# Performance work log

Measured on AMD Instinct MI355X. Metric: run time of the kernel, lower is better.

Reference implementation:

```python
import jax, jax.numpy as jnp
import numpy as np

NUM_STREAMS = 4
DIM = 256
SINKHORN_ITERS = 10
SINKHORN_TAU = 0.05


def sinkhorn_log(logits, num_iters=SINKHORN_ITERS, tau=SINKHORN_TAU):
    n = logits.shape[-1]
    z = logits / tau
    log_marginal = -jnp.log(jnp.asarray(float(n), dtype=logits.dtype))

    def body(carry, _):
        u, v = carry
        u = log_marginal - jax.scipy.special.logsumexp(z + v[None, :], axis=1)
        v = log_marginal - jax.scipy.special.logsumexp(z + u[:, None], axis=0)
        return (u, v), None

    u0 = jnp.zeros((n,), dtype=z.dtype)
    v0 = jnp.zeros((n,), dtype=z.dtype)
    (u, v), _ = jax.lax.scan(body, (u0, v0), None, length=num_iters)
    return jnp.exp(z + u[:, None] + v[None, :]) * n


def setup_inputs() -> dict:
    key = jax.random.key(0)
    k_res, k_w = jax.random.split(key)
    B = 65536
    residuals = jax.random.normal(k_res, (B, NUM_STREAMS, DIM), dtype=jnp.float32)
    # h_res_logits: -8 everywhere, 0 on diagonal (as in __init__)
    h_res_logits = jnp.full((NUM_STREAMS, NUM_STREAMS), -8.0, dtype=jnp.float32)
    h_res_logits = h_res_logits.at[jnp.arange(NUM_STREAMS), jnp.arange(NUM_STREAMS)].set(0.0)
    # h_pre_logits: -8 everywhere, 0 at init_residual_index=0
    h_pre_logits = jnp.full((NUM_STREAMS,), -8.0, dtype=jnp.float32).at[0].set(0.0)
    h_post_logits = jnp.zeros((NUM_STREAMS,), dtype=jnp.float32)
    # branch Linear(dim, dim, bias=False): weight (out, in), y = x @ W.T
    bound = 1.0 / np.sqrt(DIM)
    W_branch = jax.random.uniform(k_w, (DIM, DIM), dtype=jnp.float32, minval=-bound, maxval=bound)
    return {
        "residuals": residuals,
        "h_res_logits": h_res_logits,
        "h_pre_logits": h_pre_logits,
        "h_post_logits": h_post_logits,
        "W_branch": W_branch,
    }


def reference(residuals, h_res_logits, h_pre_logits, h_post_logits, W_branch):
    # residuals: (B, S, D)
    h_res = sinkhorn_log(h_res_logits)                     # (S, S) doubly-stochastic * n
    h_pre = jax.nn.softmax(h_pre_logits)                   # (S,)
    h_post = jax.nn.softmax(h_post_logits)                 # (S,)
    residuals_mixed = jnp.einsum('st,bsd->btd', h_res, residuals)
    branch_input = jnp.einsum('s,bsd->bd', h_pre, residuals)
    branch_output = branch_input @ W_branch.T              # (B, D)
    depth_out = jnp.einsum('bd,s->bsd', branch_output, h_post)
    return residuals_mixed + depth_out
```

## Files before the change

### kernel.cpp

```cpp
#include <hip/hip_runtime.h>

#define NSTREAMS 4
#define DIM 256
#define BM 16
#define NTHREADS 1024
#define TILES 16

typedef __attribute__((ext_vector_type(8))) short short8;
typedef __attribute__((ext_vector_type(4))) float f32x4;

static __device__ __forceinline__ int2 f2bf4(float4 v) {
    unsigned int lo, hi;
    asm("v_cvt_pk_bf16_f32 %0, %1, %2" : "=v"(lo) : "v"(v.x), "v"(v.y));
    asm("v_cvt_pk_bf16_f32 %0, %1, %2" : "=v"(hi) : "v"(v.z), "v"(v.w));
    int2 r; r.x = (int)lo; r.y = (int)hi;
    return r;
}

static __device__ __forceinline__ float rfl(float x) {
    int i = __builtin_amdgcn_readfirstlane(__builtin_bit_cast(int, x));
    return __builtin_bit_cast(float, i);
}

static __device__ __forceinline__ void barrier_lgkm() {
    asm volatile("s_waitcnt lgkmcnt(0)\n\ts_barrier" ::: "memory");
}

__global__ __launch_bounds__(NTHREADS, 1) void fused_kernel(
    const float* __restrict__ res,
    const float* __restrict__ Wb,
    const float* __restrict__ hres_l,
    const float* __restrict__ hpre_l,
    const float* __restrict__ hpost_l,
    float* __restrict__ out)
{
    __shared__ __align__(16) short bi_lds[2][BM][DIM + 8];
    __shared__ __align__(16) float bo_lds[BM][DIM + 4];

    const int t  = threadIdx.x;
    const int w  = t >> 6;
    const int l  = t & 63;
    const int lr = l & 15;
    const int lk = l >> 4;

    const long tile0 = (long)blockIdx.x * TILES;
    const long tstride = (long)BM * (NSTREAMS * DIM);
    const float* rl0 = res + (tile0 * BM + w) * (long)(NSTREAMS * DIM) + l * 4;
    float* ob0 = out + (tile0 * BM + w) * (long)(4 * DIM) + l * 4;
    const int dcol = w * 16 + lr;

    float4 A0, A1, A2, A3;
    A0 = *reinterpret_cast<const float4*>(rl0 + 0 * DIM);
    A1 = *reinterpret_cast<const float4*>(rl0 + 1 * DIM);
    A2 = *reinterpret_cast<const float4*>(rl0 + 2 * DIM);
    A3 = *reinterpret_cast<const float4*>(rl0 + 3 * DIM);

    const float4* wrow4 = reinterpret_cast<const float4*>(Wb + dcol * DIM);
    float4 wfa[8], wfb[8];
    #pragma unroll
    for (int kk = 0; kk < 8; ++kk) {
        wfa[kk] = wrow4[kk * 8 + lk * 2];
        wfb[kk] = wrow4[kk * 8 + lk * 2 + 1];
    }

    float hres[4][4];
    float hp0, hp1, hp2, hp3;
    float hq[4];
    {
        const int li = l & 15;
        float z = hres_l[li] * 20.0f;
        float uu = 0.f, vv = 0.f;
        const float logm = -logf(4.0f);
        #pragma unroll 1
        for (int it = 0; it < 10; ++it) {
            float tj = z + vv;
            float m = fmaxf(tj, __shfl_xor(tj, 1));
            m = fmaxf(m, __shfl_xor(m, 2));
            float e = expf(tj - m);
            float ss = e + __shfl_xor(e, 1);
            ss += __shfl_xor(ss, 2);
            uu = logm - (m + logf(ss));
            float ti2 = z + uu;
            float m2 = fmaxf(ti2, __shfl_xor(ti2, 4));
            m2 = fmaxf(m2, __shfl_xor(m2, 8));
            float e2 = expf(ti2 - m2);
            float s2 = e2 + __shfl_xor(e2, 4);
            s2 += __shfl_xor(s2, 8);
            vv = logm - (m2 + logf(s2));
        }
        float hval = expf(z + uu + vv) * 4.0f;
        #pragma unroll
        for (int s = 0; s < 4; ++s)
            #pragma unroll
            for (int tt = 0; tt < 4; ++tt)
                hres[s][tt] = rfl(__shfl(hval, s * 4 + tt));
        float p0 = hpre_l[0], p1 = hpre_l[1], p2 = hpre_l[2], p3 = hpre_l[3];
        float pm = fmaxf(fmaxf(p0, p1), fmaxf(p2, p3));
        float e0 = expf(p0 - pm), e1 = expf(p1 - pm), e2 = expf(p2 - pm), e3 = expf(p3 - pm);
        float es = e0 + e1 + e2 + e3;
        hp0 = rfl(e0 / es); hp1 = rfl(e1 / es); hp2 = rfl(e2 / es); hp3 = rfl(e3 / es);
        float q0 = hpost_l[0], q1 = hpost_l[1], q2 = hpost_l[2], q3 = hpost_l[3];
        float qm = fmaxf(fmaxf(q0, q1), fmaxf(q2, q3));
        float f0 = expf(q0 - qm), f1 = expf(q1 - qm), f2 = expf(q2 - qm), f3 = expf(q3 - qm);
        float fs = f0 + f1 + f2 + f3;
        hq[0] = rfl(f0 / fs); hq[1] = rfl(f1 / fs); hq[2] = rfl(f2 / fs); hq[3] = rfl(f3 / fs);
    }

    short8 wf[8];
    #pragma unroll
    for (int kk = 0; kk < 8; ++kk) {
        union { int4 i; short8 s; } u8;
        int2 lo = f2bf4(wfa[kk]);
        int2 hi = f2bf4(wfb[kk]);
        u8.i.x = lo.x; u8.i.y = lo.y; u8.i.z = hi.x; u8.i.w = hi.y;
        wf[kk] = u8.s;
    }

    {
        float4 bi;
        bi.x = hp0 * A0.x + hp1 * A1.x + hp2 * A2.x + hp3 * A3.x;
        bi.y = hp0 * A0.y + hp1 * A1.y + hp2 * A2.y + hp3 * A3.y;
        bi.z = hp0 * A0.z + hp1 * A1.z + hp2 * A2.z + hp3 * A3.z;
        bi.w = hp0 * A0.w + hp1 * A1.w + hp2 * A2.w + hp3 * A3.w;
        *reinterpret_cast<int2*>(&bi_lds[0][w][l * 4]) = f2bf4(bi);
    }
    float4 B0, B1, B2, B3;
    B0 = *reinterpret_cast<const float4*>(rl0 + tstride + 0 * DIM);
    B1 = *reinterpret_cast<const float4*>(rl0 + tstride + 1 * DIM);
    B2 = *reinterpret_cast<const float4*>(rl0 + tstride + 2 * DIM);
    B3 = *reinterpret_cast<const float4*>(rl0 + tstride + 3 * DIM);

    barrier_lgkm();

    for (int ti = 0; ti < TILES; ti += 2) {
        {
            f32x4 acc = {0.f, 0.f, 0.f, 0.f};
            #pragma unroll
            for (int kk = 0; kk < 8; ++kk) {
                short8 bfrag = *reinterpret_cast<const short8*>(&bi_lds[0][lr][kk * 32 + lk * 8]);
                acc = __builtin_amdgcn_mfma_f32_16x16x32_bf16(wf[kk], bfrag, acc, 0, 0, 0);
            }
            *reinterpret_cast<f32x4*>(&bo_lds[lr][(w << 4) + (lk << 2)]) = acc;
            barrier_lgkm();
            {
                f32x4 bo = *reinterpret_cast<const f32x4*>(&bo_lds[w][l * 4]);
                float* ob = ob0 + ti * (long)(BM * 4 * DIM);
                #pragma unroll
                for (int tt = 0; tt < 4; ++tt) {
                    float4 o;
                    o.x = hq[tt] * bo[0] + hres[0][tt] * A0.x + hres[1][tt] * A1.x + hres[2][tt] * A2.x + hres[3][tt] * A3.x;
                    o.y = hq[tt] * bo[1] + hres[0][tt] * A0.y + hres[1][tt] * A1.y + hres[2][tt] * A2.y + hres[3][tt] * A3.y;
                    o.z = hq[tt] * bo[2] + hres[0][tt] * A0.z + hres[1][tt] * A1.z + hres[2][tt] * A2.z + hres[3][tt] * A3.z;
                    o.w = hq[tt] * bo[3] + hres[0][tt] * A0.w + hres[1][tt] * A1.w + hres[2][tt] * A2.w + hres[3][tt] * A3.w;
                    *reinterpret_cast<float4*>(ob + tt * DIM) = o;
                }
            }
            if (ti + 2 < TILES) {
                const float* rb = rl0 + (ti + 2) * tstride;
                A0 = *reinterpret_cast<const float4*>(rb + 0 * DIM);
                A1 = *reinterpret_cast<const float4*>(rb + 1 * DIM);
                A2 = *reinterpret_cast<const float4*>(rb + 2 * DIM);
                A3 = *reinterpret_cast<const float4*>(rb + 3 * DIM);
            }
            __builtin_amdgcn_sched_barrier(0);
            {
                float4 bi;
                bi.x = hp0 * B0.x + hp1 * B1.x + hp2 * B2.x + hp3 * B3.x;
                bi.y = hp0 * B0.y + hp1 * B1.y + hp2 * B2.y + hp3 * B3.y;
                bi.z = hp0 * B0.z + hp1 * B1.z + hp2 * B2.z + hp3 * B3.z;
                bi.w = hp0 * B0.w + hp1 * B1.w + hp2 * B2.w + hp3 * B3.w;
                *reinterpret_cast<int2*>(&bi_lds[1][w][l * 4]) = f2bf4(bi);
            }
            barrier_lgkm();
        }
        {
            f32x4 acc = {0.f, 0.f, 0.f, 0.f};
            #pragma unroll
            for (int kk = 0; kk < 8; ++kk) {
                short8 bfrag = *reinterpret_cast<const short8*>(&bi_lds[1][lr][kk * 32 + lk * 8]);
                acc = __builtin_amdgcn_mfma_f32_16x16x32_bf16(wf[kk], bfrag, acc, 0, 0, 0);
            }
            *reinterpret_cast<f32x4*>(&bo_lds[lr][(w << 4) + (lk << 2)]) = acc;
            barrier_lgkm();
            {
                f32x4 bo = *reinterpret_cast<const f32x4*>(&bo_lds[w][l * 4]);
                float* ob = ob0 + (ti + 1) * (long)(BM * 4 * DIM);
                #pragma unroll
                for (int tt = 0; tt < 4; ++tt) {
                    float4 o;
                    o.x = hq[tt] * bo[0] + hres[0][tt] * B0.x + hres[1][tt] * B1.x + hres[2][tt] * B2.x + hres[3][tt] * B3.x;
                    o.y = hq[tt] * bo[1] + hres[0][tt] * B0.y + hres[1][tt] * B1.y + hres[2][tt] * B2.y + hres[3][tt] * B3.y;
                    o.z = hq[tt] * bo[2] + hres[0][tt] * B0.z + hres[1][tt] * B1.z + hres[2][tt] * B2.z + hres[3][tt] * B3.z;
                    o.w = hq[tt] * bo[3] + hres[0][tt] * B0.w + hres[1][tt] * B1.w + hres[2][tt] * B2.w + hres[3][tt] * B3.w;
                    *reinterpret_cast<float4*>(ob + tt * DIM) = o;
                }
            }
            if (ti + 3 < TILES) {
                const float* rb = rl0 + (ti + 3) * tstride;
                B0 = *reinterpret_cast<const float4*>(rb + 0 * DIM);
                B1 = *reinterpret_cast<const float4*>(rb + 1 * DIM);
                B2 = *reinterpret_cast<const float4*>(rb + 2 * DIM);
                B3 = *reinterpret_cast<const float4*>(rb + 3 * DIM);
            }
            __builtin_amdgcn_sched_barrier(0);
            if (ti + 2 < TILES) {
                float4 bi;
                bi.x = hp0 * A0.x + hp1 * A1.x + hp2 * A2.x + hp3 * A3.x;
                bi.y = hp0 * A0.y + hp1 * A1.y + hp2 * A2.y + hp3 * A3.y;
                bi.z = hp0 * A0.z + hp1 * A1.z + hp2 * A2.z + hp3 * A3.z;
                bi.w = hp0 * A0.w + hp1 * A1.w + hp2 * A2.w + hp3 * A3.w;
                *reinterpret_cast<int2*>(&bi_lds[0][w][l * 4]) = f2bf4(bi);
            }
            barrier_lgkm();
        }
    }
}

extern "C" void kernel_launch(void* const* d_in, const int* in_sizes, int n_in,
                              void* d_out, int out_size, void* d_ws, size_t ws_size,
                              hipStream_t stream) {
    const float* res     = (const float*)d_in[0];
    const float* hres_l  = (const float*)d_in[1];
    const float* hpre_l  = (const float*)d_in[2];
    const float* hpost_l = (const float*)d_in[3];
    const float* Wb      = (const float*)d_in[4];
    float* out = (float*)d_out;

    const int Btot = in_sizes[0] / (NSTREAMS * DIM);
    const int grid = Btot / (BM * TILES);

    fused_kernel<<<grid, NTHREADS, 0, stream>>>(
        res, Wb, hres_l, hpre_l, hpost_l, out);
}
```

Measured before the change: 114.4 us.

## Software-pipeline MFMA and epilogue with double-buffered output LDS to halve barriers

Double-buffers the branch-output LDS tile so the epilogue for tile i-1 runs in the same phase as the MFMA for tile i. This drops one block-wide barrier per tile. The residual-mix part of each output (hres times the four streams) is now computed early, when the residuals are loaded, and held in registers, so the epilogue only adds hq*bo. This adds about 32 live VGPRs (opA/opB) and LDS usage, which could raise register pressure in the 1024-thread block.

```diff
diff --git a/kernel.cpp b/kernel.cpp
--- a/kernel.cpp
+++ b/kernel.cpp
@@ -35,7 +35,7 @@
     float* __restrict__ out)
 {
     __shared__ __align__(16) short bi_lds[2][BM][DIM + 8];
-    __shared__ __align__(16) float bo_lds[BM][DIM + 4];
+    __shared__ __align__(16) float bo_lds[2][BM][DIM + 4];
 
     const int t  = threadIdx.x;
     const int w  = t >> 6;
@@ -116,6 +116,7 @@
         wf[kk] = u8.s;
     }
 
+    float4 opA[4], opB[4];
     {
         float4 bi;
         bi.x = hp0 * A0.x + hp1 * A1.x + hp2 * A2.x + hp3 * A3.x;
@@ -123,6 +124,13 @@
         bi.z = hp0 * A0.z + hp1 * A1.z + hp2 * A2.z + hp3 * A3.z;
         bi.w = hp0 * A0.w + hp1 * A1.w + hp2 * A2.w + hp3 * A3.w;
         *reinterpret_cast<int2*>(&bi_lds[0][w][l * 4]) = f2bf4(bi);
+        #pragma unroll
+        for (int tt = 0; tt < 4; ++tt) {
+            opA[tt].x = hres[0][tt] * A0.x + hres[1][tt] * A1.x + hres[2][tt] * A2.x + hres[3][tt] * A3.x;
+            opA[tt].y = hres[0][tt] * A0.y + hres[1][tt] * A1.y + hres[2][tt] * A2.y + hres[3][tt] * A3.y;
+            opA[tt].z = hres[0][tt] * A0.z + hres[1][tt] * A1.z + hres[2][tt] * A2.z + hres[3][tt] * A3.z;
+            opA[tt].w = hres[0][tt] * A0.w + hres[1][tt] * A1.w + hres[2][tt] * A2.w + hres[3][tt] * A3.w;
+        }
     }
     float4 B0, B1, B2, B3;
     B0 = *reinterpret_cast<const float4*>(rl0 + tstride + 0 * DIM);
@@ -134,27 +142,6 @@
 
     for (int ti = 0; ti < TILES; ti += 2) {
         {
-            f32x4 acc = {0.f, 0.f, 0.f, 0.f};
-            #pragma unroll
-            for (int kk = 0; kk < 8; ++kk) {
-                short8 bfrag = *reinterpret_cast<const short8*>(&bi_lds[0][lr][kk * 32 + lk * 8]);
-                acc = __builtin_amdgcn_mfma_f32_16x16x32_bf16(wf[kk], bfrag, acc, 0, 0, 0);
-            }
-            *reinterpret_cast<f32x4*>(&bo_lds[lr][(w << 4) + (lk << 2)]) = acc;
-            barrier_lgkm();
-            {
-                f32x4 bo = *reinterpret_cast<const f32x4*>(&bo_lds[w][l * 4]);
-                float* ob = ob0 + ti * (long)(BM * 4 * DIM);
-                #pragma unroll
-                for (int tt = 0; tt < 4; ++tt) {
-                    float4 o;
-                    o.x = hq[tt] * bo[0] + hres[0][tt] * A0.x + hres[1][tt] * A1.x + hres[2][tt] * A2.x + hres[3][tt] * A3.x;
-                    o.y = hq[tt] * bo[1] + hres[0][tt] * A0.y + hres[1][tt] * A1.y + hres[2][tt] * A2.y + hres[3][tt] * A3.y;
-                    o.z = hq[tt] * bo[2] + hres[0][tt] * A0.z + hres[1][tt] * A1.z + hres[2][tt] * A2.z + hres[3][tt] * A3.z;
-                    o.w = hq[tt] * bo[3] + hres[0][tt] * A0.w + hres[1][tt] * A1.w + hres[2][tt] * A2.w + hres[3][tt] * A3.w;
-                    *reinterpret_cast<float4*>(ob + tt * DIM) = o;
-                }
-            }
             if (ti + 2 < TILES) {
                 const float* rb = rl0 + (ti + 2) * tstride;
                 A0 = *reinterpret_cast<const float4*>(rb + 0 * DIM);
@@ -163,6 +150,28 @@
                 A3 = *reinterpret_cast<const float4*>(rb + 3 * DIM);
             }
             __builtin_amdgcn_sched_barrier(0);
+            if (ti > 0) {
+                f32x4 bo = *reinterpret_cast<const f32x4*>(&bo_lds[1][w][l * 4]);
+                float* ob = ob0 + (ti - 1) * (long)(BM * 4 * DIM);
+                #pragma unroll
+                for (int tt = 0; tt < 4; ++tt) {
+                    float4 o;
+                    o.x = opB[tt].x + hq[tt] * bo[0];
+                    o.y = opB[tt].y + hq[tt] * bo[1];
+                    o.z = opB[tt].z + hq[tt] * bo[2];
+                    o.w = opB[tt].w + hq[tt] * bo[3];
+                    *reinterpret_cast<float4*>(ob + tt * DIM) = o;
+                }
+            }
+            {
+                f32x4 acc = {0.f, 0.f, 0.f, 0.f};
+                #pragma unroll
+                for (int kk = 0; kk < 8; ++kk) {
+                    short8 bfrag = *reinterpret_cast<const short8*>(&bi_lds[0][lr][kk * 32 + lk * 8]);
+                    acc = __builtin_amdgcn_mfma_f32_16x16x32_bf16(wf[kk], bfrag, acc, 0, 0, 0);
+                }
+                *reinterpret_cast<f32x4*>(&bo_lds[0][lr][(w << 4) + (lk << 2)]) = acc;
+            }
             {
                 float4 bi;
                 bi.x = hp0 * B0.x + hp1 * B1.x + hp2 * B2.x + hp3 * B3.x;
@@ -170,31 +179,17 @@
                 bi.z = hp0 * B0.z + hp1 * B1.z + hp2 * B2.z + hp3 * B3.z;
                 bi.w = hp0 * B0.w + hp1 * B1.w + hp2 * B2.w + hp3 * B3.w;
                 *reinterpret_cast<int2*>(&bi_lds[1][w][l * 4]) = f2bf4(bi);
+                #pragma unroll
+                for (int tt = 0; tt < 4; ++tt) {
+                    opB[tt].x = hres[0][tt] * B0.x + hres[1][tt] * B1.x + hres[2][tt] * B2.x + hres[3][tt] * B3.x;
+                    opB[tt].y = hres[0][tt] * B0.y + hres[1][tt] * B1.y + hres[2][tt] * B2.y + hres[3][tt] * B3.y;
+                    opB[tt].z = hres[0][tt] * B0.z + hres[1][tt] * B1.z + hres[2][tt] * B2.z + hres[3][tt] * B3.z;
+                    opB[tt].w = hres[0][tt] * B0.w + hres[1][tt] * B1.w + hres[2][tt] * B2.w + hres[3][tt] * B3.w;
+                }
             }
             barrier_lgkm();
         }
         {
-            f32x4 acc = {0.f, 0.f, 0.f, 0.f};
-            #pragma unroll
-            for (int kk = 0; kk < 8; ++kk) {
-                short8 bfrag = *reinterpret_cast<const short8*>(&bi_lds[1][lr][kk * 32 + lk * 8]);
-                acc = __builtin_amdgcn_mfma_f32_16x16x32_bf16(wf[kk], bfrag, acc, 0, 0, 0);
-            }
-            *reinterpret_cast<f32x4*>(&bo_lds[lr][(w << 4) + (lk << 2)]) = acc;
-            barrier_lgkm();
-            {
-                f32x4 bo = *reinterpret_cast<const f32x4*>(&bo_lds[w][l * 4]);
-                float* ob = ob0 + (ti + 1) * (long)(BM * 4 * DIM);
-                #pragma unroll
-                for (int tt = 0; tt < 4; ++tt) {
-                    float4 o;
-                    o.x = hq[tt] * bo[0] + hres[0][tt] * B0.x + hres[1][tt] * B1.x + hres[2][tt] * B2.x + hres[3][tt] * B3.x;
-                    o.y = hq[tt] * bo[1] + hres[0][tt] * B0.y + hres[1][tt] * B1.y + hres[2][tt] * B2.y + hres[3][tt] * B3.y;
-                    o.z = hq[tt] * bo[2] + hres[0][tt] * B0.z + hres[1][tt] * B1.z + hres[2][tt] * B2.z + hres[3][tt] * B3.z;
-                    o.w = hq[tt] * bo[3] + hres[0][tt] * B0.w + hres[1][tt] * B1.w + hres[2][tt] * B2.w + hres[3][tt] * B3.w;
-                    *reinterpret_cast<float4*>(ob + tt * DIM) = o;
-                }
-            }
             if (ti + 3 < TILES) {
                 const float* rb = rl0 + (ti + 3) * tstride;
                 B0 = *reinterpret_cast<const float4*>(rb + 0 * DIM);
@@ -203,6 +198,28 @@
                 B3 = *reinterpret_cast<const float4*>(rb + 3 * DIM);
             }
             __builtin_amdgcn_sched_barrier(0);
+            {
+                f32x4 bo = *reinterpret_cast<const f32x4*>(&bo_lds[0][w][l * 4]);
+                float* ob = ob0 + ti * (long)(BM * 4 * DIM);
+                #pragma unroll
+                for (int tt = 0; tt < 4; ++tt) {
+                    float4 o;
+                    o.x = opA[tt].x + hq[tt] * bo[0];
+                    o.y = opA[tt].y + hq[tt] * bo[1];
+                    o.z = opA[tt].z + hq[tt] * bo[2];
+                    o.w = opA[tt].w + hq[tt] * bo[3];
+                    *reinterpret_cast<float4*>(ob + tt * DIM) = o;
+                }
+            }
+            {
+                f32x4 acc = {0.f, 0.f, 0.f, 0.f};
+                #pragma unroll
+                for (int kk = 0; kk < 8; ++kk) {
+                    short8 bfrag = *reinterpret_cast<const short8*>(&bi_lds[1][lr][kk * 32 + lk * 8]);
+                    acc = __builtin_amdgcn_mfma_f32_16x16x32_bf16(wf[kk], bfrag, acc, 0, 0, 0);
+                }
+                *reinterpret_cast<f32x4*>(&bo_lds[1][lr][(w << 4) + (lk << 2)]) = acc;
+            }
             if (ti + 2 < TILES) {
                 float4 bi;
                 bi.x = hp0 * A0.x + hp1 * A1.x + hp2 * A2.x + hp3 * A3.x;
@@ -210,8 +227,28 @@
                 bi.z = hp0 * A0.z + hp1 * A1.z + hp2 * A2.z + hp3 * A3.z;
                 bi.w = hp0 * A0.w + hp1 * A1.w + hp2 * A2.w + hp3 * A3.w;
                 *reinterpret_cast<int2*>(&bi_lds[0][w][l * 4]) = f2bf4(bi);
+                #pragma unroll
+                for (int tt = 0; tt < 4; ++tt) {
+                    opA[tt].x = hres[0][tt] * A0.x + hres[1][tt] * A1.x + hres[2][tt] * A2.x + hres[3][tt] * A3.x;
+                    opA[tt].y = hres[0][tt] * A0.y + hres[1][tt] * A1.y + hres[2][tt] * A2.y + hres[3][tt] * A3.y;
+                    opA[tt].z = hres[0][tt] * A0.z + hres[1][tt] * A1.z + hres[2][tt] * A2.z + hres[3][tt] * A3.z;
+                    opA[tt].w = hres[0][tt] * A0.w + hres[1][tt] * A1.w + hres[2][tt] * A2.w + hres[3][tt] * A3.w;
+                }
             }
             barrier_lgkm();
+        }
+    }
+    {
+        f32x4 bo = *reinterpret_cast<const f32x4*>(&bo_lds[1][w][l * 4]);
+        float* ob = ob0 + (TILES - 1) * (long)(BM * 4 * DIM);
+        #pragma unroll
+        for (int tt = 0; tt < 4; ++tt) {
+            float4 o;
+            o.x = opB[tt].x + hq[tt] * bo[0];
+            o.y = opB[tt].y + hq[tt] * bo[1];
+            o.z = opB[tt].z + hq[tt] * bo[2];
+            o.w = opB[tt].w + hq[tt] * bo[3];
+            *reinterpret_cast<float4*>(ob + tt * DIM) = o;
         }
     }
 }
```

Result: slower. 124.2 us (+8.6%).

## Drop register-resident weights and double buffering, raise occupancy with smaller tiles

Applied to the files above, without the earlier changes.

The kernel no longer preloads and converts the branch weight fragments into registers once per block. It now reloads them from global memory and converts them to bf16 inside every MFMA k-step. The two-stage register/LDS double-buffered pipeline becomes a simple single-buffer loop, TILES per block drops from 16 to 8 (twice the blocks), and launch bounds now ask for 8 blocks per CU instead of 1. The aim is to cut register pressure so more waves can hide memory latency, at the cost of redundant weight loads and conversions on every tile and no explicit prefetch overlap.

```diff
diff --git a/kernel.cpp b/kernel.cpp
--- a/kernel.cpp
+++ b/kernel.cpp
@@ -4,7 +4,7 @@
 #define DIM 256
 #define BM 16
 #define NTHREADS 1024
-#define TILES 16
+#define TILES 8
 
 typedef __attribute__((ext_vector_type(8))) short short8;
 typedef __attribute__((ext_vector_type(4))) float f32x4;
@@ -26,7 +26,7 @@
     asm volatile("s_waitcnt lgkmcnt(0)\n\ts_barrier" ::: "memory");
 }
 
-__global__ __launch_bounds__(NTHREADS, 1) void fused_kernel(
+__global__ __launch_bounds__(NTHREADS, 8) void fused_kernel(
     const float* __restrict__ res,
     const float* __restrict__ Wb,
     const float* __restrict__ hres_l,
@@ -34,7 +34,7 @@
     const float* __restrict__ hpost_l,
     float* __restrict__ out)
 {
-    __shared__ __align__(16) short bi_lds[2][BM][DIM + 8];
+    __shared__ __align__(16) short bi_lds[BM][DIM + 8];
     __shared__ __align__(16) float bo_lds[BM][DIM + 4];
 
     const int t  = threadIdx.x;
@@ -48,20 +48,7 @@
     const float* rl0 = res + (tile0 * BM + w) * (long)(NSTREAMS * DIM) + l * 4;
     float* ob0 = out + (tile0 * BM + w) * (long)(4 * DIM) + l * 4;
     const int dcol = w * 16 + lr;
-
-    float4 A0, A1, A2, A3;
-    A0 = *reinterpret_cast<const float4*>(rl0 + 0 * DIM);
-    A1 = *reinterpret_cast<const float4*>(rl0 + 1 * DIM);
-    A2 = *reinterpret_cast<const float4*>(rl0 + 2 * DIM);
-    A3 = *reinterpret_cast<const float4*>(rl0 + 3 * DIM);
-
     const float4* wrow4 = reinterpret_cast<const float4*>(Wb + dcol * DIM);
-    float4 wfa[8], wfb[8];
-    #pragma unroll
-    for (int kk = 0; kk < 8; ++kk) {
-        wfa[kk] = wrow4[kk * 8 + lk * 2];
-        wfb[kk] = wrow4[kk * 8 + lk * 2 + 1];
-    }
 
     float hres[4][4];
     float hp0, hp1, hp2, hp3;
@@ -106,112 +93,52 @@
         hq[0] = rfl(f0 / fs); hq[1] = rfl(f1 / fs); hq[2] = rfl(f2 / fs); hq[3] = rfl(f3 / fs);
     }
 
-    short8 wf[8];
-    #pragma unroll
-    for (int kk = 0; kk < 8; ++kk) {
-        union { int4 i; short8 s; } u8;
-        int2 lo = f2bf4(wfa[kk]);
-        int2 hi = f2bf4(wfb[kk]);
-        u8.i.x = lo.x; u8.i.y = lo.y; u8.i.z = hi.x; u8.i.w = hi.y;
-        wf[kk] = u8.s;
-    }
+    for (int ti = 0; ti < TILES; ++ti) {
+        const float* rb = rl0 + ti * tstride;
+        float4 R0 = *reinterpret_cast<const float4*>(rb + 0 * DIM);
+        float4 R1 = *reinterpret_cast<const float4*>(rb + 1 * DIM);
+        float4 R2 = *reinterpret_cast<const float4*>(rb + 2 * DIM);
+        float4 R3 = *reinterpret_cast<const float4*>(rb + 3 * DIM);
 
-    {
-        float4 bi;
-        bi.x = hp0 * A0.x + hp1 * A1.x + hp2 * A2.x + hp3 * A3.x;
-        bi.y = hp0 * A0.y + hp1 * A1.y + hp2 * A2.y + hp3 * A3.y;
-        bi.z = hp0 * A0.z + hp1 * A1.z + hp2 * A2.z + hp3 * A3.z;
-        bi.w = hp0 * A0.w + hp1 * A1.w + hp2 * A2.w + hp3 * A3.w;
-        *reinterpret_cast<int2*>(&bi_lds[0][w][l * 4]) = f2bf4(bi);
-    }
-    float4 B0, B1, B2, B3;
-    B0 = *reinterpret_cast<const float4*>(rl0 + tstride + 0 * DIM);
-    B1 = *reinterpret_cast<const float4*>(rl0 + tstride + 1 * DIM);
-    B2 = *reinterpret_cast<const float4*>(rl0 + tstride + 2 * DIM);
-    B3 = *reinterpret_cast<const float4*>(rl0 + tstride + 3 * DIM);
+        {
+            float4 bi;
+            bi.x = hp0 * R0.x + hp1 * R1.x + hp2 * R2.x + hp3 * R3.x;
+            bi.y = hp0 * R0.y + hp1 * R1.y + hp2 * R2.y + hp3 * R3.y;
+            bi.z = hp0 * R0.z + hp1 * R1.z + hp2 * R2.z + hp3 * R3.z;
+            bi.w = hp0 * R0.w + hp1 * R1.w + hp2 * R2.w + hp3 * R3.w;
+            *reinterpret_cast<int2*>(&bi_lds[w][l * 4]) = f2bf4(bi);
+        }
+        barrier_lgkm();
 
-    barrier_lgkm();
-
-    for (int ti = 0; ti < TILES; ti += 2) {
         {
             f32x4 acc = {0.f, 0.f, 0.f, 0.f};
             #pragma unroll
             for (int kk = 0; kk < 8; ++kk) {
-                short8 bfrag = *reinterpret_cast<const short8*>(&bi_lds[0][lr][kk * 32 + lk * 8]);
-                acc = __builtin_amdgcn_mfma_f32_16x16x32_bf16(wf[kk], bfrag, acc, 0, 0, 0);
+                short8 bfrag = *reinterpret_cast<const short8*>(&bi_lds[lr][kk * 32 + lk * 8]);
+                float4 wa = wrow4[kk * 8 + lk * 2];
+                float4 wb2 = wrow4[kk * 8 + lk * 2 + 1];
+                union { int4 i; short8 s; } u8;
+                int2 lo = f2bf4(wa);
+                int2 hi = f2bf4(wb2);
+                u8.i.x = lo.x; u8.i.y = lo.y; u8.i.z = hi.x; u8.i.w = hi.y;
+                acc = __builtin_amdgcn_mfma_f32_16x16x32_bf16(u8.s, bfrag, acc, 0, 0, 0);
             }
             *reinterpret_cast<f32x4*>(&bo_lds[lr][(w << 4) + (lk << 2)]) = acc;
-            barrier_lgkm();
-            {
-                f32x4 bo = *reinterpret_cast<const f32x4*>(&bo_lds[w][l * 4]);
-                float* ob = ob0 + ti * (long)(BM * 4 * DIM);
-                #pragma unroll
-                for (int tt = 0; tt < 4; ++tt) {
-                    float4 o;
-                    o.x = hq[tt] * bo[0] + hres[0][tt] * A0.x + hres[1][tt] * A1.x + hres[2][tt] * A2.x + hres[3][tt] * A3.x;
-                    o.y = hq[tt] * bo[1] + hres[0][tt] * A0.y + hres[1][tt] * A1.y + hres[2][tt] * A2.y + hres[3][tt] * A3.y;
-                    o.z = hq[tt] * bo[2] + hres[0][tt] * A0.z + hres[1][tt] * A1.z + hres[2][tt] * A2.z + hres[3][tt] * A3.z;
-                    o.w = hq[tt] * bo[3] + hres[0][tt] * A0.w + hres[1][tt] * A1.w + hres[2][tt] * A2.w + hres[3][tt] * A3.w;
-                    *reinterpret_cast<float4*>(ob + tt * DIM) = o;
-                }
+        }
+        barrier_lgkm();
+
+        {
+            f32x4 bo = *reinterpret_cast<const f32x4*>(&bo_lds[w][l * 4]);
+            float* ob = ob0 + ti * (long)(BM * 4 * DIM);
+            #pragma unroll
+            for (int tt = 0; tt < 4; ++tt) {
+                float4 o;
+                o.x = hq[tt] * bo[0] + hres[0][tt] * R0.x + hres[1][tt] * R1.x + hres[2][tt] * R2.x + hres[3][tt] * R3.x;
+                o.y = hq[tt] * bo[1] + hres[0][tt] * R0.y + hres[1][tt] * R1.y + hres[2][tt] * R2.y + hres[3][tt] * R3.y;
+                o.z = hq[tt] * bo[2] + hres[0][tt] * R0.z + hres[1][tt] * R1.z + hres[2][tt] * R2.z + hres[3][tt] * R3.z;
+                o.w = hq[tt] * bo[3] + hres[0][tt] * R0.w + hres[1][tt] * R1.w + hres[2][tt] * R2.w + hres[3][tt] * R3.w;
+                *reinterpret_cast<float4*>(ob + tt * DIM) = o;
             }
-            if (ti + 2 < TILES) {
-                const float* rb = rl0 + (ti + 2) * tstride;
-                A0 = *reinterpret_cast<const float4*>(rb + 0 * DIM);
-                A1 = *reinterpret_cast<const float4*>(rb + 1 * DIM);
-                A2 = *reinterpret_cast<const float4*>(rb + 2 * DIM);
-                A3 = *reinterpret_cast<const float4*>(rb + 3 * DIM);
-            }
-            __builtin_amdgcn_sched_barrier(0);
-            {
-                float4 bi;
-                bi.x = hp0 * B0.x + hp1 * B1.x + hp2 * B2.x + hp3 * B3.x;
-                bi.y = hp0 * B0.y + hp1 * B1.y + hp2 * B2.y + hp3 * B3.y;
-                bi.z = hp0 * B0.z + hp1 * B1.z + hp2 * B2.z + hp3 * B3.z;
-                bi.w = hp0 * B0.w + hp1 * B1.w + hp2 * B2.w + hp3 * B3.w;
-                *reinterpret_cast<int2*>(&bi_lds[1][w][l * 4]) = f2bf4(bi);
-            }
-            barrier_lgkm();
-        }
-        {
-            f32x4 acc = {0.f, 0.f, 0.f, 0.f};
-            #pragma unroll
-            for (int kk = 0; kk < 8; ++kk) {
-                short8 bfrag = *reinterpret_cast<const short8*>(&bi_lds[1][lr][kk * 32 + lk * 8]);
-                acc = __builtin_amdgcn_mfma_f32_16x16x32_bf16(wf[kk], bfrag, acc, 0, 0, 0);
-            }
-            *reinterpret_cast<f32x4*>(&bo_lds[lr][(w << 4) + (lk << 2)]) = acc;
-            barrier_lgkm();
-            {
-                f32x4 bo = *reinterpret_cast<const f32x4*>(&bo_lds[w][l * 4]);
-                float* ob = ob0 + (ti + 1) * (long)(BM * 4 * DIM);
-                #pragma unroll
-                for (int tt = 0; tt < 4; ++tt) {
-                    float4 o;
-                    o.x = hq[tt] * bo[0] + hres[0][tt] * B0.x + hres[1][tt] * B1.x + hres[2][tt] * B2.x + hres[3][tt] * B3.x;
-                    o.y = hq[tt] * bo[1] + hres[0][tt] * B0.y + hres[1][tt] * B1.y + hres[2][tt] * B2.y + hres[3][tt] * B3.y;
-                    o.z = hq[tt] * bo[2] + hres[0][tt] * B0.z + hres[1][tt] * B1.z + hres[2][tt] * B2.z + hres[3][tt] * B3.z;
-                    o.w = hq[tt] * bo[3] + hres[0][tt] * B0.w + hres[1][tt] * B1.w + hres[2][tt] * B2.w + hres[3][tt] * B3.w;
-                    *reinterpret_cast<float4*>(ob + tt * DIM) = o;
-                }
-            }
-            if (ti + 3 < TILES) {
-                const float* rb = rl0 + (ti + 3) * tstride;
-                B0 = *reinterpret_cast<const float4*>(rb + 0 * DIM);
-                B1 = *reinterpret_cast<const float4*>(rb + 1 * DIM);
-                B2 = *reinterpret_cast<const float4*>(rb + 2 * DIM);
-                B3 = *reinterpret_cast<const float4*>(rb + 3 * DIM);
-            }
-            __builtin_amdgcn_sched_barrier(0);
-            if (ti + 2 < TILES) {
-                float4 bi;
-                bi.x = hp0 * A0.x + hp1 * A1.x + hp2 * A2.x + hp3 * A3.x;
-                bi.y = hp0 * A0.y + hp1 * A1.y + hp2 * A2.y + hp3 * A3.y;
-                bi.z = hp0 * A0.z + hp1 * A1.z + hp2 * A2.z + hp3 * A3.z;
-                bi.w = hp0 * A0.w + hp1 * A1.w + hp2 * A2.w + hp3 * A3.w;
-                *reinterpret_cast<int2*>(&bi_lds[0][w][l * 4]) = f2bf4(bi);
-            }
-            barrier_lgkm();
         }
     }
 }
```

Result: slower. 191.9 us (+67.8%).
